# Kernel tuning notes

Hardware: AMD Instinct MI355X
Metric: run time of the kernel (lower is better)

## Reference

```python
import jax, jax.numpy as jnp
import numpy as np

D_MODEL = 1024
N_HEADS = 16
D_K = D_MODEL // N_HEADS
B, S = 2, 2048


def setup_inputs() -> dict:
    key = jax.random.key(0)
    ks = jax.random.split(key, 5)
    x = jax.random.normal(ks[0], (B, S, D_MODEL), dtype=jnp.float32)
    # causal 0/1 mask, broadcastable over batch and heads
    mask = jnp.tril(jnp.ones((S, S), dtype=jnp.int32))[None, None, :, :]
    scale = 1.0 / np.sqrt(D_MODEL)
    w_qkv_w = jax.random.normal(ks[1], (3 * D_MODEL, D_MODEL), dtype=jnp.float32) * scale
    w_qkv_b = jnp.zeros((3 * D_MODEL,), dtype=jnp.float32)
    w_o_w = jax.random.normal(ks[2], (D_MODEL, D_MODEL), dtype=jnp.float32) * scale
    w_o_b = jnp.zeros((D_MODEL,), dtype=jnp.float32)
    return {"x": x, "mask": mask, "w_qkv_w": w_qkv_w, "w_qkv_b": w_qkv_b,
            "w_o_w": w_o_w, "w_o_b": w_o_b}


def reference(x, mask, w_qkv_w, w_qkv_b, w_o_w, w_o_b):
    b, s, d = x.shape
    qkv = x @ w_qkv_w.T + w_qkv_b                       # [b, s, 3d]
    q, k, v = jnp.split(qkv, 3, axis=-1)
    # [b, h, s, dk]
    q = q.reshape(b, s, N_HEADS, D_K).transpose(0, 2, 1, 3)
    k = k.reshape(b, s, N_HEADS, D_K).transpose(0, 2, 1, 3)
    v = v.reshape(b, s, N_HEADS, D_K).transpose(0, 2, 1, 3)
    scores = jnp.einsum('bhqd,bhkd->bhqk', q, k) / jnp.sqrt(jnp.float32(D_K))
    scores = jnp.where(mask == 0, jnp.float32(-1e9), scores)
    attn = jax.nn.softmax(scores, axis=-1)
    out = jnp.einsum('bhqk,bhkd->bhqd', attn, v)        # [b, h, s, dk]
    out = out.transpose(0, 2, 1, 3).reshape(b, s, d)
    return out @ w_o_w.T + w_o_b
```

## Files before the change

kernel.cpp:

```cpp
#include <hip/hip_runtime.h>
#include <cstdint>
#include <cstddef>


typedef __attribute__((ext_vector_type(8))) short bf16x8;
typedef __attribute__((ext_vector_type(4))) float f32x4;
typedef __attribute__((ext_vector_type(4))) unsigned int u32x4;
typedef __attribute__((ext_vector_type(4))) unsigned short u16x4;
typedef __attribute__((ext_vector_type(8))) unsigned short u16x8;

__device__ __forceinline__ unsigned short f2b(float f) {
  unsigned int u = __float_as_uint(f);
  u = u + 0x7FFFu + ((u >> 16) & 1u);
  return (unsigned short)(u >> 16);
}
__device__ __forceinline__ unsigned short f2b_trunc(float f) {
  return (unsigned short)(__float_as_uint(f) >> 16);
}

__device__ __forceinline__ void gl_lds16(const unsigned short* g, unsigned short* s) {
  __builtin_amdgcn_global_load_lds((const __attribute__((address_space(1))) void*)g,
                                   (__attribute__((address_space(3))) void*)s, 16, 0, 0);
}

__global__ __launch_bounds__(256) void cvt_all(const float* __restrict__ x,
                                               const float* __restrict__ wq,
                                               const float* __restrict__ wo,
                                               unsigned short* __restrict__ xb,
                                               unsigned short* __restrict__ wqb,
                                               unsigned short* __restrict__ wob) {
  const int bid = blockIdx.x;
  const float* in;
  unsigned short* out;
  int base;
  if (bid < 4096)      { in = x;  out = xb;  base = bid; }
  else if (bid < 7168) { in = wq; out = wqb; base = bid - 4096; }
  else                 { in = wo; out = wob; base = bid - 7168; }
  const int idx = (base * 256 + threadIdx.x) * 4;
  f32x4 v = *(const f32x4*)(in + idx);
  u16x4 r;
  r[0] = f2b(v[0]); r[1] = f2b(v[1]); r[2] = f2b(v[2]); r[3] = f2b(v[3]);
  *(u16x4*)(out + idx) = r;
}

__global__ __launch_bounds__(256) void gemm_bt(const unsigned short* __restrict__ A,
                                               const unsigned short* __restrict__ W,
                                               const float* __restrict__ bias,
                                               unsigned short* __restrict__ Cb,
                                               int M, int N, int K, int qcols) {
  __shared__ unsigned short As[128 * 64];
  __shared__ unsigned short Bs[128 * 64];
  const int tid  = threadIdx.x;
  const int lane = tid & 63;
  const int w    = tid >> 6;
  const int wy   = w >> 1, wx = w & 1;
  const int l15  = lane & 15, quad = lane >> 4;
  const int xr   = l15 & 7;
  const int m0 = blockIdx.y * 128, n0 = blockIdx.x * 128;

  const unsigned short* gA[4];
  const unsigned short* gB[4];
  unsigned short* sA[4];
  unsigned short* sB[4];
#pragma unroll
  for (int p = 0; p < 4; ++p) {
    const int c = tid + p * 256;
    const int r = c >> 3;
    const int srcc = (c & 7) ^ (r & 7);
    gA[p] = A + (size_t)(m0 + r) * K + srcc * 8;
    gB[p] = W + (size_t)(n0 + r) * K + srcc * 8;
    sA[p] = &As[c * 8];
    sB[p] = &Bs[c * 8];
  }

  f32x4 acc[4][4];
#pragma unroll
  for (int i = 0; i < 4; ++i)
#pragma unroll
    for (int j = 0; j < 4; ++j) acc[i][j] = (f32x4){0.f, 0.f, 0.f, 0.f};

  for (int kt = 0; kt < K; kt += 64) {
#pragma unroll
    for (int p = 0; p < 4; ++p) {
      gl_lds16(gA[p] + kt, sA[p]);
      gl_lds16(gB[p] + kt, sB[p]);
    }
    __syncthreads();
#pragma unroll
    for (int kc = 0; kc < 2; ++kc) {
      bf16x8 af[4], bfr[4];
#pragma unroll
      for (int i = 0; i < 4; ++i)
        af[i] = *(const bf16x8*)&As[(wy * 64 + i * 16 + l15) * 64 + ((kc * 4 + quad) ^ xr) * 8];
#pragma unroll
      for (int j = 0; j < 4; ++j)
        bfr[j] = *(const bf16x8*)&Bs[(wx * 64 + j * 16 + l15) * 64 + ((kc * 4 + quad) ^ xr) * 8];
#pragma unroll
      for (int i = 0; i < 4; ++i)
#pragma unroll
        for (int j = 0; j < 4; ++j)
          acc[i][j] = __builtin_amdgcn_mfma_f32_16x16x32_bf16(af[i], bfr[j], acc[i][j], 0, 0, 0);
    }
    __syncthreads();
  }

#pragma unroll
  for (int i = 0; i < 4; ++i) {
    const int row = m0 + wy * 64 + i * 16 + quad * 4;
#pragma unroll
    for (int j = 0; j < 4; ++j) {
      const int col = n0 + wx * 64 + j * 16 + l15;
      const float bv = bias[col];
      const float sc = (col < qcols) ? 0.125f : 1.0f;
#pragma unroll
      for (int r = 0; r < 4; ++r)
        Cb[(size_t)(row + r) * N + col] = f2b((acc[i][j][r] + bv) * sc);
    }
  }
}

__global__ __launch_bounds__(256) void gemm_bt64(const unsigned short* __restrict__ A,
                                                 const unsigned short* __restrict__ W,
                                                 const float* __restrict__ bias,
                                                 float* __restrict__ Cf,
                                                 int M, int N, int K) {
  __shared__ unsigned short As[64 * 64];
  __shared__ unsigned short Bs[128 * 64];
  const int tid  = threadIdx.x;
  const int lane = tid & 63;
  const int w    = tid >> 6;
  const int wy   = w >> 1, wx = w & 1;
  const int l15  = lane & 15, quad = lane >> 4;
  const int xr   = l15 & 7;
  const int m0 = blockIdx.y * 64, n0 = blockIdx.x * 128;

  const unsigned short* gA[2];
  const unsigned short* gB[4];
  unsigned short* sA[2];
  unsigned short* sB[4];
#pragma unroll
  for (int p = 0; p < 2; ++p) {
    const int c = tid + p * 256;
    const int r = c >> 3;
    const int srcc = (c & 7) ^ (r & 7);
    gA[p] = A + (size_t)(m0 + r) * K + srcc * 8;
    sA[p] = &As[c * 8];
  }
#pragma unroll
  for (int p = 0; p < 4; ++p) {
    const int c = tid + p * 256;
    const int r = c >> 3;
    const int srcc = (c & 7) ^ (r & 7);
    gB[p] = W + (size_t)(n0 + r) * K + srcc * 8;
    sB[p] = &Bs[c * 8];
  }

  f32x4 acc[2][4];
#pragma unroll
  for (int i = 0; i < 2; ++i)
#pragma unroll
    for (int j = 0; j < 4; ++j) acc[i][j] = (f32x4){0.f, 0.f, 0.f, 0.f};

  for (int kt = 0; kt < K; kt += 64) {
#pragma unroll
    for (int p = 0; p < 2; ++p) gl_lds16(gA[p] + kt, sA[p]);
#pragma unroll
    for (int p = 0; p < 4; ++p) gl_lds16(gB[p] + kt, sB[p]);
    __syncthreads();
#pragma unroll
    for (int kc = 0; kc < 2; ++kc) {
      bf16x8 af[2], bfr[4];
#pragma unroll
      for (int i = 0; i < 2; ++i)
        af[i] = *(const bf16x8*)&As[(wy * 32 + i * 16 + l15) * 64 + ((kc * 4 + quad) ^ xr) * 8];
#pragma unroll
      for (int j = 0; j < 4; ++j)
        bfr[j] = *(const bf16x8*)&Bs[(wx * 64 + j * 16 + l15) * 64 + ((kc * 4 + quad) ^ xr) * 8];
#pragma unroll
      for (int i = 0; i < 2; ++i)
#pragma unroll
        for (int j = 0; j < 4; ++j)
          acc[i][j] = __builtin_amdgcn_mfma_f32_16x16x32_bf16(af[i], bfr[j], acc[i][j], 0, 0, 0);
    }
    __syncthreads();
  }

#pragma unroll
  for (int i = 0; i < 2; ++i) {
    const int row = m0 + wy * 32 + i * 16 + quad * 4;
#pragma unroll
    for (int j = 0; j < 4; ++j) {
      const int col = n0 + wx * 64 + j * 16 + l15;
      const float bv = bias[col];
#pragma unroll
      for (int r = 0; r < 4; ++r)
        Cf[(size_t)(row + r) * N + col] = acc[i][j][r] + bv;
    }
  }
}

__global__ __launch_bounds__(256) void transpose_v(const unsigned short* __restrict__ qkv,
                                                   unsigned short* __restrict__ vt) {
  __shared__ unsigned short tile[64][72];
  const int tid = threadIdx.x;
  const int bh = blockIdx.y, b = bh >> 4, h = bh & 15;
  const int s0 = blockIdx.x * 64;
  const int i = tid >> 2;
  const int j = (tid & 3) * 16;
  const unsigned short* g = qkv + (size_t)(b * 2048 + s0 + i) * 3072 + 2048 + h * 64 + j;
  *(u32x4*)&tile[i][j]     = *(const u32x4*)g;
  *(u32x4*)&tile[i][j + 8] = *(const u32x4*)(g + 8);
  __syncthreads();
  const int d  = tid >> 2;
  const int sj = (tid & 3) * 16;
  u16x8 o0, o1;
#pragma unroll
  for (int k = 0; k < 8; ++k) { o0[k] = tile[sj + k][d]; o1[k] = tile[sj + 8 + k][d]; }
  unsigned short* gout = vt + (size_t)(bh * 64 + d) * 2048 + s0 + sj;
  *(u16x8*)gout       = o0;
  *(u16x8*)(gout + 8) = o1;
}

__global__ __launch_bounds__(256) void attn_fwd(const unsigned short* __restrict__ qkv,
                                                const unsigned short* __restrict__ vt,
                                                unsigned short* __restrict__ o) {
  __shared__ unsigned short Ks[2][64 * 72];
  __shared__ unsigned short Vs[2][64 * 72];
  __shared__ unsigned short pbuf[4][16 * 72];
  const int tid  = threadIdx.x;
  const int lane = tid & 63;
  const int w    = tid >> 6;
  const int l15  = lane & 15, quad = lane >> 4;
  const int bh = blockIdx.x, b = bh >> 4, h = bh & 15;
  const int qtile = 31 - (int)blockIdx.y;
  const int q0 = qtile * 64 + w * 16;
  const int T = qtile + 1;

  const int srow = tid >> 2;
  const int scol = (tid & 3) * 16;
  const unsigned short* gK = qkv + (size_t)(b * 2048 + srow) * 3072 + 1024 + h * 64 + scol;
  const unsigned short* gV = vt + (size_t)(bh * 64 + srow) * 2048 + scol;

  const unsigned short* qbase = qkv + (size_t)(b * 2048 + q0 + l15) * 3072 + h * 64;
  const bf16x8 aq0 = *(const bf16x8*)(qbase + quad * 8);
  const bf16x8 aq1 = *(const bf16x8*)(qbase + 32 + quad * 8);

  bf16x8 vones;
#pragma unroll
  for (int k = 0; k < 8; ++k) vones[k] = (short)0x3F80;

  f32x4 acc[4];
#pragma unroll
  for (int j = 0; j < 4; ++j) acc[j] = (f32x4){0.f, 0.f, 0.f, 0.f};
  f32x4 accL = (f32x4){0.f, 0.f, 0.f, 0.f};

  unsigned short* P = pbuf[w];

  {
    u32x4 k0 = *(const u32x4*)gK, k1 = *(const u32x4*)(gK + 8);
    u32x4 v0 = *(const u32x4*)gV, v1 = *(const u32x4*)(gV + 8);
    unsigned short* sK = &Ks[0][srow * 72 + scol];
    unsigned short* sV = &Vs[0][srow * 72 + scol];
    *(u32x4*)sK = k0; *(u32x4*)(sK + 8) = k1;
    *(u32x4*)sV = v0; *(u32x4*)(sV + 8) = v1;
  }

  for (int t = 0; t < T; ++t) {
    __syncthreads();
    const int cur = t & 1;
    const unsigned short* Kc = Ks[cur];
    const unsigned short* Vc = Vs[cur];
    u32x4 nk0, nk1, nv0, nv1;
    const bool more = (t + 1 < T);
    if (more) {
      const size_t ko = (size_t)(t + 1) * 64 * 3072;
      const int vo = (t + 1) * 64;
      nk0 = *(const u32x4*)(gK + ko); nk1 = *(const u32x4*)(gK + ko + 8);
      nv0 = *(const u32x4*)(gV + vo); nv1 = *(const u32x4*)(gV + vo + 8);
    }
    const int kv0 = t * 64;
    f32x4 s[4];
#pragma unroll
    for (int n = 0; n < 4; ++n) {
      const bf16x8 bk0 = *(const bf16x8*)&Kc[(n * 16 + l15) * 72 + quad * 8];
      const bf16x8 bk1 = *(const bf16x8*)&Kc[(n * 16 + l15) * 72 + 32 + quad * 8];
      f32x4 z = (f32x4){0.f, 0.f, 0.f, 0.f};
      z = __builtin_amdgcn_mfma_f32_16x16x32_bf16(aq0, bk0, z, 0, 0, 0);
      z = __builtin_amdgcn_mfma_f32_16x16x32_bf16(aq1, bk1, z, 0, 0, 0);
      s[n] = z;
    }
    if (kv0 + 63 > q0) {
#pragma unroll
      for (int n = 0; n < 4; ++n)
#pragma unroll
        for (int r = 0; r < 4; ++r)
          if (kv0 + n * 16 + l15 > q0 + quad * 4 + r) s[n][r] = -1e30f;
    }
#pragma unroll
    for (int n = 0; n < 4; ++n)
#pragma unroll
      for (int r = 0; r < 4; ++r) s[n][r] = __expf(s[n][r]);
#pragma unroll
    for (int n = 0; n < 4; ++n)
#pragma unroll
      for (int r = 0; r < 4; ++r)
        P[(quad * 4 + r) * 72 + n * 16 + l15] = f2b_trunc(s[n][r]);
    const bf16x8 ap0 = *(const bf16x8*)&P[l15 * 72 + quad * 8];
    const bf16x8 ap1 = *(const bf16x8*)&P[l15 * 72 + 32 + quad * 8];
#pragma unroll
    for (int j = 0; j < 4; ++j) {
      const bf16x8 bv0 = *(const bf16x8*)&Vc[(j * 16 + l15) * 72 + quad * 8];
      const bf16x8 bv1 = *(const bf16x8*)&Vc[(j * 16 + l15) * 72 + 32 + quad * 8];
      acc[j] = __builtin_amdgcn_mfma_f32_16x16x32_bf16(ap0, bv0, acc[j], 0, 0, 0);
      acc[j] = __builtin_amdgcn_mfma_f32_16x16x32_bf16(ap1, bv1, acc[j], 0, 0, 0);
    }
    accL = __builtin_amdgcn_mfma_f32_16x16x32_bf16(ap0, vones, accL, 0, 0, 0);
    accL = __builtin_amdgcn_mfma_f32_16x16x32_bf16(ap1, vones, accL, 0, 0, 0);
    if (more) {
      unsigned short* sK = &Ks[cur ^ 1][srow * 72 + scol];
      unsigned short* sV = &Vs[cur ^ 1][srow * 72 + scol];
      *(u32x4*)sK = nk0; *(u32x4*)(sK + 8) = nk1;
      *(u32x4*)sV = nv0; *(u32x4*)(sV + 8) = nv1;
    }
  }
#pragma unroll
  for (int j = 0; j < 4; ++j)
#pragma unroll
    for (int r = 0; r < 4; ++r) {
      const float v = acc[j][r] / accL[r];
      o[(size_t)(b * 2048 + q0 + quad * 4 + r) * 1024 + h * 64 + j * 16 + l15] = f2b(v);
    }
}

extern "C" void kernel_launch(void* const* d_in, const int* in_sizes, int n_in,
                              void* d_out, int out_size, void* d_ws, size_t ws_size,
                              hipStream_t stream) {
  const float* x       = (const float*)d_in[0];
  const float* w_qkv_w = (const float*)d_in[2];
  const float* w_qkv_b = (const float*)d_in[3];
  const float* w_o_w   = (const float*)d_in[4];
  const float* w_o_b   = (const float*)d_in[5];
  float* out = (float*)d_out;

  unsigned short* ws    = (unsigned short*)d_ws;
  unsigned short* xb    = ws;
  unsigned short* wqb   = xb   + (size_t)4096 * 1024;
  unsigned short* wob   = wqb  + (size_t)3072 * 1024;
  unsigned short* qkvb  = wob  + (size_t)1024 * 1024;
  unsigned short* vtb   = qkvb + (size_t)4096 * 3072;
  unsigned short* attnb = vtb  + (size_t)2048 * 2048;

  cvt_all<<<8192, 256, 0, stream>>>(x, w_qkv_w, w_o_w, xb, wqb, wob);
  gemm_bt<<<dim3(24, 32), 256, 0, stream>>>(xb, wqb, w_qkv_b, qkvb, 4096, 3072, 1024, 1024);
  transpose_v<<<dim3(32, 32), 256, 0, stream>>>(qkvb, vtb);
  attn_fwd<<<dim3(32, 32), 256, 0, stream>>>(qkvb, vtb, attnb);
  gemm_bt64<<<dim3(8, 64), 256, 0, stream>>>(attnb, wob, w_o_b, out, 4096, 1024, 1024);
}
```

Baseline: 198.9 us.

## Process 128 queries per attention block, two 16-row tiles per wave

Each attention block now covers 128 query rows instead of 64, with each wave handling two 16-row query subtiles. This halves the grid and reuses every K/V tile loaded into shared memory across twice as many queries, cutting K/V global traffic and load overhead. The MFMA operands are swapped to compute the transposed score tile, which allows vectorized P stores and output writes, and launch bounds request two blocks per SM. Costs are higher register pressure, more work in the diagonal tiles, and fewer blocks for load balancing across the causal triangle.

```diff
diff --git a/kernel.cpp b/kernel.cpp
--- a/kernel.cpp
+++ b/kernel.cpp
@@ -221,38 +221,44 @@
   *(u16x8*)(gout + 8) = o1;
 }
 
-__global__ __launch_bounds__(256) void attn_fwd(const unsigned short* __restrict__ qkv,
-                                                const unsigned short* __restrict__ vt,
-                                                unsigned short* __restrict__ o) {
+__global__ __launch_bounds__(256, 2) void attn_fwd(const unsigned short* __restrict__ qkv,
+                                                   const unsigned short* __restrict__ vt,
+                                                   unsigned short* __restrict__ o) {
   __shared__ unsigned short Ks[2][64 * 72];
   __shared__ unsigned short Vs[2][64 * 72];
-  __shared__ unsigned short pbuf[4][16 * 72];
+  __shared__ unsigned short pbuf[4][32 * 72];
   const int tid  = threadIdx.x;
   const int lane = tid & 63;
   const int w    = tid >> 6;
   const int l15  = lane & 15, quad = lane >> 4;
   const int bh = blockIdx.x, b = bh >> 4, h = bh & 15;
-  const int qtile = 31 - (int)blockIdx.y;
-  const int q0 = qtile * 64 + w * 16;
-  const int T = qtile + 1;
+  const int qt = 15 - (int)blockIdx.y;
+  const int q0 = qt * 128;
+  const int qa = q0 + w * 32;
+  const int qb = qa + 16;
+  const int T = 2 * qt + 2;
 
   const int srow = tid >> 2;
   const int scol = (tid & 3) * 16;
   const unsigned short* gK = qkv + (size_t)(b * 2048 + srow) * 3072 + 1024 + h * 64 + scol;
   const unsigned short* gV = vt + (size_t)(bh * 64 + srow) * 2048 + scol;
 
-  const unsigned short* qbase = qkv + (size_t)(b * 2048 + q0 + l15) * 3072 + h * 64;
-  const bf16x8 aq0 = *(const bf16x8*)(qbase + quad * 8);
-  const bf16x8 aq1 = *(const bf16x8*)(qbase + 32 + quad * 8);
+  const unsigned short* qra = qkv + (size_t)(b * 2048 + qa + l15) * 3072 + h * 64;
+  const unsigned short* qrb = qkv + (size_t)(b * 2048 + qb + l15) * 3072 + h * 64;
+  const bf16x8 bq[2][2] = {
+    { *(const bf16x8*)(qra + quad * 8), *(const bf16x8*)(qra + 32 + quad * 8) },
+    { *(const bf16x8*)(qrb + quad * 8), *(const bf16x8*)(qrb + 32 + quad * 8) } };
 
   bf16x8 vones;
 #pragma unroll
   for (int k = 0; k < 8; ++k) vones[k] = (short)0x3F80;
 
-  f32x4 acc[4];
-#pragma unroll
-  for (int j = 0; j < 4; ++j) acc[j] = (f32x4){0.f, 0.f, 0.f, 0.f};
-  f32x4 accL = (f32x4){0.f, 0.f, 0.f, 0.f};
+  f32x4 acc[2][4];
+#pragma unroll
+  for (int i = 0; i < 2; ++i)
+#pragma unroll
+    for (int j = 0; j < 4; ++j) acc[i][j] = (f32x4){0.f, 0.f, 0.f, 0.f};
+  f32x4 accL[2] = {(f32x4){0.f, 0.f, 0.f, 0.f}, (f32x4){0.f, 0.f, 0.f, 0.f}};
 
   unsigned short* P = pbuf[w];
 
@@ -279,43 +285,60 @@
       nv0 = *(const u32x4*)(gV + vo); nv1 = *(const u32x4*)(gV + vo + 8);
     }
     const int kv0 = t * 64;
-    f32x4 s[4];
+
+    f32x4 st[2][4];
 #pragma unroll
     for (int n = 0; n < 4; ++n) {
-      const bf16x8 bk0 = *(const bf16x8*)&Kc[(n * 16 + l15) * 72 + quad * 8];
-      const bf16x8 bk1 = *(const bf16x8*)&Kc[(n * 16 + l15) * 72 + 32 + quad * 8];
-      f32x4 z = (f32x4){0.f, 0.f, 0.f, 0.f};
-      z = __builtin_amdgcn_mfma_f32_16x16x32_bf16(aq0, bk0, z, 0, 0, 0);
-      z = __builtin_amdgcn_mfma_f32_16x16x32_bf16(aq1, bk1, z, 0, 0, 0);
-      s[n] = z;
-    }
-    if (kv0 + 63 > q0) {
-#pragma unroll
-      for (int n = 0; n < 4; ++n)
-#pragma unroll
-        for (int r = 0; r < 4; ++r)
-          if (kv0 + n * 16 + l15 > q0 + quad * 4 + r) s[n][r] = -1e30f;
-    }
-#pragma unroll
-    for (int n = 0; n < 4; ++n)
-#pragma unroll
-      for (int r = 0; r < 4; ++r) s[n][r] = __expf(s[n][r]);
-#pragma unroll
-    for (int n = 0; n < 4; ++n)
-#pragma unroll
-      for (int r = 0; r < 4; ++r)
-        P[(quad * 4 + r) * 72 + n * 16 + l15] = f2b_trunc(s[n][r]);
-    const bf16x8 ap0 = *(const bf16x8*)&P[l15 * 72 + quad * 8];
-    const bf16x8 ap1 = *(const bf16x8*)&P[l15 * 72 + 32 + quad * 8];
+      const bf16x8 kA0 = *(const bf16x8*)&Kc[(n * 16 + l15) * 72 + quad * 8];
+      const bf16x8 kA1 = *(const bf16x8*)&Kc[(n * 16 + l15) * 72 + 32 + quad * 8];
+      f32x4 z0 = (f32x4){0.f, 0.f, 0.f, 0.f};
+      z0 = __builtin_amdgcn_mfma_f32_16x16x32_bf16(kA0, bq[0][0], z0, 0, 0, 0);
+      z0 = __builtin_amdgcn_mfma_f32_16x16x32_bf16(kA1, bq[0][1], z0, 0, 0, 0);
+      st[0][n] = z0;
+      f32x4 z1 = (f32x4){0.f, 0.f, 0.f, 0.f};
+      z1 = __builtin_amdgcn_mfma_f32_16x16x32_bf16(kA0, bq[1][0], z1, 0, 0, 0);
+      z1 = __builtin_amdgcn_mfma_f32_16x16x32_bf16(kA1, bq[1][1], z1, 0, 0, 0);
+      st[1][n] = z1;
+    }
+#pragma unroll
+    for (int tq = 0; tq < 2; ++tq) {
+      const int qbase = tq ? qb : qa;
+      if (kv0 + 63 > qbase) {
+        const int qrow = qbase + l15;
+#pragma unroll
+        for (int n = 0; n < 4; ++n)
+#pragma unroll
+          for (int r = 0; r < 4; ++r)
+            if (kv0 + n * 16 + quad * 4 + r > qrow) st[tq][n][r] = -1e30f;
+      }
+#pragma unroll
+      for (int n = 0; n < 4; ++n) {
+#pragma unroll
+        for (int r = 0; r < 4; ++r) st[tq][n][r] = __expf(st[tq][n][r]);
+        u16x4 pw;
+        pw[0] = f2b_trunc(st[tq][n][0]); pw[1] = f2b_trunc(st[tq][n][1]);
+        pw[2] = f2b_trunc(st[tq][n][2]); pw[3] = f2b_trunc(st[tq][n][3]);
+        *(u16x4*)&P[(tq * 16 + l15) * 72 + n * 16 + quad * 4] = pw;
+      }
+    }
+    bf16x8 av[4][2];
 #pragma unroll
     for (int j = 0; j < 4; ++j) {
-      const bf16x8 bv0 = *(const bf16x8*)&Vc[(j * 16 + l15) * 72 + quad * 8];
-      const bf16x8 bv1 = *(const bf16x8*)&Vc[(j * 16 + l15) * 72 + 32 + quad * 8];
-      acc[j] = __builtin_amdgcn_mfma_f32_16x16x32_bf16(ap0, bv0, acc[j], 0, 0, 0);
-      acc[j] = __builtin_amdgcn_mfma_f32_16x16x32_bf16(ap1, bv1, acc[j], 0, 0, 0);
-    }
-    accL = __builtin_amdgcn_mfma_f32_16x16x32_bf16(ap0, vones, accL, 0, 0, 0);
-    accL = __builtin_amdgcn_mfma_f32_16x16x32_bf16(ap1, vones, accL, 0, 0, 0);
+      av[j][0] = *(const bf16x8*)&Vc[(j * 16 + l15) * 72 + quad * 8];
+      av[j][1] = *(const bf16x8*)&Vc[(j * 16 + l15) * 72 + 32 + quad * 8];
+    }
+#pragma unroll
+    for (int tq = 0; tq < 2; ++tq) {
+      const bf16x8 bp0 = *(const bf16x8*)&P[(tq * 16 + l15) * 72 + quad * 8];
+      const bf16x8 bp1 = *(const bf16x8*)&P[(tq * 16 + l15) * 72 + 32 + quad * 8];
+      accL[tq] = __builtin_amdgcn_mfma_f32_16x16x32_bf16(vones, bp0, accL[tq], 0, 0, 0);
+      accL[tq] = __builtin_amdgcn_mfma_f32_16x16x32_bf16(vones, bp1, accL[tq], 0, 0, 0);
+#pragma unroll
+      for (int j = 0; j < 4; ++j) {
+        acc[tq][j] = __builtin_amdgcn_mfma_f32_16x16x32_bf16(av[j][0], bp0, acc[tq][j], 0, 0, 0);
+        acc[tq][j] = __builtin_amdgcn_mfma_f32_16x16x32_bf16(av[j][1], bp1, acc[tq][j], 0, 0, 0);
+      }
+    }
     if (more) {
       unsigned short* sK = &Ks[cur ^ 1][srow * 72 + scol];
       unsigned short* sV = &Vs[cur ^ 1][srow * 72 + scol];
@@ -324,12 +347,18 @@
     }
   }
 #pragma unroll
-  for (int j = 0; j < 4; ++j)
-#pragma unroll
-    for (int r = 0; r < 4; ++r) {
-      const float v = acc[j][r] / accL[r];
-      o[(size_t)(b * 2048 + q0 + quad * 4 + r) * 1024 + h * 64 + j * 16 + l15] = f2b(v);
-    }
+  for (int tq = 0; tq < 2; ++tq) {
+    const int qrow = (tq ? qb : qa) + l15;
+    const float inv = 1.0f / accL[tq][0];
+    unsigned short* orow = o + (size_t)(b * 2048 + qrow) * 1024 + h * 64;
+#pragma unroll
+    for (int j = 0; j < 4; ++j) {
+      u16x4 ov;
+      ov[0] = f2b(acc[tq][j][0] * inv); ov[1] = f2b(acc[tq][j][1] * inv);
+      ov[2] = f2b(acc[tq][j][2] * inv); ov[3] = f2b(acc[tq][j][3] * inv);
+      *(u16x4*)(orow + j * 16 + quad * 4) = ov;
+    }
+  }
 }
 
 extern "C" void kernel_launch(void* const* d_in, const int* in_sizes, int n_in,
@@ -353,6 +382,6 @@
   cvt_all<<<8192, 256, 0, stream>>>(x, w_qkv_w, w_o_w, xb, wqb, wob);
   gemm_bt<<<dim3(24, 32), 256, 0, stream>>>(xb, wqb, w_qkv_b, qkvb, 4096, 3072, 1024, 1024);
   transpose_v<<<dim3(32, 32), 256, 0, stream>>>(qkvb, vtb);
-  attn_fwd<<<dim3(32, 32), 256, 0, stream>>>(qkvb, vtb, attnb);
+  attn_fwd<<<dim3(32, 16), 256, 0, stream>>>(qkvb, vtb, attnb);
   gemm_bt64<<<dim3(8, 64), 256, 0, stream>>>(attnb, wob, w_o_b, out, 4096, 1024, 1024);
 }
```

Measured after the change: 201.1 us. About the same (+1.1%).
